# Kernel optimization log

Hardware: AMD Instinct MI355X
Metric: run time of the kernel (lower is better)

Reference implementation:

```python
import jax, jax.numpy as jnp
import numpy as np

SCALE = 128.0  # init arg; divisor is sqrt(scale)
NEG_BIG = -1e10

def setup_inputs() -> dict:
    key = jax.random.key(0)
    kq, kk, kv, km = jax.random.split(key, 4)
    B, Nq, Nk, D = 16, 2048, 2048, 128
    q = jax.random.normal(kq, (B, Nq, D), dtype=jnp.float32)
    k = jax.random.normal(kk, (B, Nk, D), dtype=jnp.float32)
    v = jax.random.normal(kv, (B, Nk, D), dtype=jnp.float32)
    mask = jax.random.randint(km, (B, Nq, Nk), 0, 2).astype(bool)
    return {"q": q, "k": k, "v": v, "mask": mask}

def reference(q, k, v, mask):
    inv = 1.0 / np.sqrt(SCALE).astype(np.float32)
    # scores: [b, q, k]
    scores = jnp.einsum('bqd,bkd->bqk', q, k) * inv
    scores = jnp.where(mask, NEG_BIG, scores)
    att = jax.nn.softmax(scores, axis=-1)
    context = jnp.einsum('bqk,bkd->bqd', att, v)
    return (context, att)
```

## Files before the change

### kernel.cpp

```cpp
#include <hip/hip_runtime.h>

#define B_ 16
#define NQ 2048
#define NK 2048
#define DH 128
#define INV 0.08838834764831843f

typedef __attribute__((ext_vector_type(8))) short bf16x8;
typedef __attribute__((ext_vector_type(4))) float f32x4;

__device__ __forceinline__ unsigned short f2b(float f) {
  unsigned u = __float_as_uint(f);
  u += 0x7fff + ((u >> 16) & 1);
  return (unsigned short)(u >> 16);
}

__global__ __launch_bounds__(256) void k_cvt(
    const float* __restrict__ src, unsigned short* __restrict__ dst, int n4) {
  int i = blockIdx.x * 256 + threadIdx.x;
  if (i >= n4) return;
  float4 f = ((const float4*)src)[i];
  ushort4 u;
  u.x = f2b(f.x); u.y = f2b(f.y); u.z = f2b(f.z); u.w = f2b(f.w);
  ((ushort4*)dst)[i] = u;
}

__global__ __launch_bounds__(256) void k_trans(
    const float* __restrict__ v, unsigned short* __restrict__ vt) {
  __shared__ float tile[32][33];
  const int b = blockIdx.z, kv0 = blockIdx.x << 5, d0 = blockIdx.y << 5;
  const int tx = threadIdx.x & 31, ty = threadIdx.x >> 5;
  #pragma unroll
  for (int i = 0; i < 4; i++)
    tile[ty + 8*i][tx] = v[((size_t)b*NK + kv0 + ty + 8*i)*DH + d0 + tx];
  __syncthreads();
  #pragma unroll
  for (int i = 0; i < 4; i++)
    vt[((size_t)b*DH + d0 + ty + 8*i)*NK + kv0 + tx] = f2b(tile[tx][ty + 8*i]);
}

__global__ __launch_bounds__(256) void k_attn(
    const unsigned short* __restrict__ qb, const unsigned short* __restrict__ kb,
    const unsigned short* __restrict__ vtb, const int* __restrict__ mask,
    float* __restrict__ att, float* __restrict__ ctx) {
  __shared__ unsigned short Qs[64][136];
  __shared__ unsigned short Ks[64][136];
  __shared__ unsigned short Vs[128][72];
  __shared__ unsigned short Ps[64][72];
  __shared__ unsigned int   Mb[64][65];
  __shared__ float Lrow[64];

  const int t = threadIdx.x;
  const int wave = t >> 6, lane = t & 63, quad = lane >> 4, l15 = lane & 15;
  const int b = blockIdx.y, q0 = blockIdx.x << 6;
  const int qh = wave >> 1, nh = wave & 1;

  const unsigned short* qg = qb  + ((size_t)b*NQ + q0)*DH;
  const unsigned short* kg = kb  + (size_t)b*NK*DH;
  const unsigned short* vg = vtb + (size_t)b*DH*NK;
  const int*   mg   = mask + ((size_t)b*NQ + q0)*NK;
  float*       attg = att  + ((size_t)b*NQ + q0)*NK;

  {
    int r = t >> 2, c = (t & 3) << 5;
    const unsigned short* src = qg + (size_t)r*DH + c;
    #pragma unroll
    for (int i = 0; i < 4; i++)
      *(uint4*)&Qs[r][c + 8*i] = *(const uint4*)(src + 8*i);
  }
  if (t < 64) Lrow[t] = 0.f;

  float lsum[8] = {0,0,0,0,0,0,0,0};

  for (int k0 = 0; k0 < NK; k0 += 64) {
    int mreg[2][2][4];
    #pragma unroll
    for (int mt = 0; mt < 2; mt++)
      #pragma unroll
      for (int nt = 0; nt < 2; nt++)
        #pragma unroll
        for (int r = 0; r < 4; r++) {
          int row = qh*32 + mt*16 + quad*4 + r;
          int col = k0 + nh*32 + nt*16 + l15;
          mreg[mt][nt][r] = mg[(size_t)row*NK + col];
        }
    __syncthreads();
    { int r = t >> 2, c = (t & 3) << 5;
      const unsigned short* src = kg + (size_t)(k0 + r)*DH + c;
      #pragma unroll
      for (int i = 0; i < 4; i++)
        *(uint4*)&Ks[r][c + 8*i] = *(const uint4*)(src + 8*i);
    }
    __syncthreads();
    f32x4 sa00 = 0, sa01 = 0, sa10 = 0, sa11 = 0;
    #pragma unroll
    for (int kd = 0; kd < 4; kd++) {
      bf16x8 a0 = *(const bf16x8*)&Qs[qh*32      + l15][kd*32 + quad*8];
      bf16x8 a1 = *(const bf16x8*)&Qs[qh*32 + 16 + l15][kd*32 + quad*8];
      bf16x8 b0 = *(const bf16x8*)&Ks[nh*32      + l15][kd*32 + quad*8];
      bf16x8 b1 = *(const bf16x8*)&Ks[nh*32 + 16 + l15][kd*32 + quad*8];
      sa00 = __builtin_amdgcn_mfma_f32_16x16x32_bf16(a0, b0, sa00, 0, 0, 0);
      sa01 = __builtin_amdgcn_mfma_f32_16x16x32_bf16(a0, b1, sa01, 0, 0, 0);
      sa10 = __builtin_amdgcn_mfma_f32_16x16x32_bf16(a1, b0, sa10, 0, 0, 0);
      sa11 = __builtin_amdgcn_mfma_f32_16x16x32_bf16(a1, b1, sa11, 0, 0, 0);
    }
    #pragma unroll
    for (int mt = 0; mt < 2; mt++)
      #pragma unroll
      for (int nt = 0; nt < 2; nt++) {
        const f32x4 s = mt ? (nt ? sa11 : sa10) : (nt ? sa01 : sa00);
        #pragma unroll
        for (int r = 0; r < 4; r++) {
          bool mm = mreg[mt][nt][r] != 0;
          unsigned long long bal = __ballot(mm);
          if (l15 == 0) {
            int row = qh*32 + mt*16 + quad*4 + r;
            ((unsigned short*)&Mb[0][0])[row*130 + (k0>>4) + nh*2 + nt] =
                (unsigned short)(bal >> (quad*16));
          }
          float p = mm ? 0.f : __expf(s[r]*INV);
          lsum[mt*4 + r] += p;
        }
      }
  }
  __syncthreads();
  #pragma unroll
  for (int j = 0; j < 8; j++)
    atomicAdd(&Lrow[qh*32 + (j>>2)*16 + quad*4 + (j&3)], lsum[j]);
  __syncthreads();
  float il[8];
  #pragma unroll
  for (int j = 0; j < 8; j++)
    il[j] = 1.0f / Lrow[qh*32 + (j>>2)*16 + quad*4 + (j&3)];

  f32x4 ca[2][4];
  #pragma unroll
  for (int i = 0; i < 2; i++)
    #pragma unroll
    for (int j = 0; j < 4; j++) ca[i][j] = 0;

  for (int k0 = 0; k0 < NK; k0 += 64) {
    __syncthreads();
    { int r = t >> 2, c = (t & 3) << 5;
      const unsigned short* src = kg + (size_t)(k0 + r)*DH + c;
      #pragma unroll
      for (int i = 0; i < 4; i++)
        *(uint4*)&Ks[r][c + 8*i] = *(const uint4*)(src + 8*i);
      int d = t >> 1, c2 = (t & 1) << 5;
      const unsigned short* vsrc = vg + (size_t)d*NK + k0 + c2;
      #pragma unroll
      for (int i = 0; i < 4; i++)
        *(uint4*)&Vs[d][c2 + 8*i] = *(const uint4*)(vsrc + 8*i);
    }
    __syncthreads();
    f32x4 sa00 = 0, sa01 = 0, sa10 = 0, sa11 = 0;
    #pragma unroll
    for (int kd = 0; kd < 4; kd++) {
      bf16x8 a0 = *(const bf16x8*)&Qs[qh*32      + l15][kd*32 + quad*8];
      bf16x8 a1 = *(const bf16x8*)&Qs[qh*32 + 16 + l15][kd*32 + quad*8];
      bf16x8 b0 = *(const bf16x8*)&Ks[nh*32      + l15][kd*32 + quad*8];
      bf16x8 b1 = *(const bf16x8*)&Ks[nh*32 + 16 + l15][kd*32 + quad*8];
      sa00 = __builtin_amdgcn_mfma_f32_16x16x32_bf16(a0, b0, sa00, 0, 0, 0);
      sa01 = __builtin_amdgcn_mfma_f32_16x16x32_bf16(a0, b1, sa01, 0, 0, 0);
      sa10 = __builtin_amdgcn_mfma_f32_16x16x32_bf16(a1, b0, sa10, 0, 0, 0);
      sa11 = __builtin_amdgcn_mfma_f32_16x16x32_bf16(a1, b1, sa11, 0, 0, 0);
    }
    #pragma unroll
    for (int mt = 0; mt < 2; mt++)
      #pragma unroll
      for (int nt = 0; nt < 2; nt++) {
        const f32x4 s = mt ? (nt ? sa11 : sa10) : (nt ? sa01 : sa00);
        #pragma unroll
        for (int r = 0; r < 4; r++) {
          int row  = qh*32 + mt*16 + quad*4 + r;
          int coll = nh*32 + nt*16 + l15;
          unsigned w = Mb[row][(k0>>5) + nh];
          int bit = (w >> (nt*16 + l15)) & 1;
          float p = bit ? 0.f : __expf(s[r]*INV) * il[mt*4 + r];
          attg[(size_t)row*NK + k0 + coll] = p;
          Ps[row][coll] = f2b(p);
        }
      }
    __syncthreads();
    #pragma unroll
    for (int kv = 0; kv < 2; kv++) {
      bf16x8 pa0 = *(const bf16x8*)&Ps[qh*32      + l15][kv*32 + quad*8];
      bf16x8 pa1 = *(const bf16x8*)&Ps[qh*32 + 16 + l15][kv*32 + quad*8];
      #pragma unroll
      for (int dt = 0; dt < 4; dt++) {
        bf16x8 vb = *(const bf16x8*)&Vs[nh*64 + dt*16 + l15][kv*32 + quad*8];
        ca[0][dt] = __builtin_amdgcn_mfma_f32_16x16x32_bf16(pa0, vb, ca[0][dt], 0, 0, 0);
        ca[1][dt] = __builtin_amdgcn_mfma_f32_16x16x32_bf16(pa1, vb, ca[1][dt], 0, 0, 0);
      }
    }
  }

  float* cg = ctx + ((size_t)b*NQ + q0)*DH;
  #pragma unroll
  for (int mt = 0; mt < 2; mt++)
    #pragma unroll
    for (int dt = 0; dt < 4; dt++)
      #pragma unroll
      for (int r = 0; r < 4; r++) {
        int row = qh*32 + mt*16 + quad*4 + r;
        int col = nh*64 + dt*16 + l15;
        cg[(size_t)row*DH + col] = ca[mt][dt][r];
      }
}

extern "C" void kernel_launch(void* const* d_in, const int* in_sizes, int n_in,
                              void* d_out, int out_size, void* d_ws, size_t ws_size,
                              hipStream_t stream) {
  const float* q = (const float*)d_in[0];
  const float* k = (const float*)d_in[1];
  const float* v = (const float*)d_in[2];
  const int* mask = (const int*)d_in[3];
  float* ctx = (float*)d_out;
  float* att = ctx + (size_t)B_*NQ*DH;

  const size_t NE = (size_t)B_*NQ*DH;
  unsigned short* qws = (unsigned short*)d_ws;
  unsigned short* kws = qws + NE;
  unsigned short* vws = kws + NE;

  k_cvt  <<<(int)(NE/1024), 256, 0, stream>>>(q, qws, (int)(NE/4));
  k_cvt  <<<(int)(NE/1024), 256, 0, stream>>>(k, kws, (int)(NE/4));
  k_trans<<<dim3(NK/32, DH/32, B_), 256, 0, stream>>>(v, vws);
  k_attn <<<dim3(NQ/64, B_), 256, 0, stream>>>(qws, kws, vws, mask, att, ctx);
}
```

Baseline: 603.2 us.

## Pipeline attention kernel with async global-to-LDS loads, swizzled LDS and smaller query tiles

Rewrites the attention kernel to use 32-row query tiles and keep Q fragments in registers. K and V tiles are staged into XOR-swizzled LDS via global_load_lds and double-buffered with explicit vmcnt waits, so loads overlap the MFMA work. The mask bits are packed into shift registers instead of an LDS bitmap, and mask loads and att stores become nontemporal. It also remaps block IDs for locality, raises occupancy via launch bounds, and adds setprio around the MFMAs. Hand-written waitcnt and barrier sequencing adds correctness risk.

```diff
diff --git a/kernel.cpp b/kernel.cpp
--- a/kernel.cpp
+++ b/kernel.cpp
@@ -9,10 +9,17 @@
 typedef __attribute__((ext_vector_type(8))) short bf16x8;
 typedef __attribute__((ext_vector_type(4))) float f32x4;
 
+typedef const __attribute__((address_space(1))) unsigned int* gas1_t;
+typedef __attribute__((address_space(3))) unsigned int* las3_t;
+
 __device__ __forceinline__ unsigned short f2b(float f) {
   unsigned u = __float_as_uint(f);
   u += 0x7fff + ((u >> 16) & 1);
   return (unsigned short)(u >> 16);
+}
+
+__device__ __forceinline__ void gl_lds16(const unsigned short* g, unsigned short* l) {
+  __builtin_amdgcn_global_load_lds((gas1_t)g, (las3_t)l, 16, 0, 0);
 }
 
 __global__ __launch_bounds__(256) void k_cvt(
@@ -39,173 +46,209 @@
     vt[((size_t)b*DH + d0 + ty + 8*i)*NK + kv0 + tx] = f2b(tile[tx][ty + 8*i]);
 }
 
-__global__ __launch_bounds__(256) void k_attn(
+__global__ __launch_bounds__(256, 4) void k_attn(
     const unsigned short* __restrict__ qb, const unsigned short* __restrict__ kb,
     const unsigned short* __restrict__ vtb, const int* __restrict__ mask,
     float* __restrict__ att, float* __restrict__ ctx) {
-  __shared__ unsigned short Qs[64][136];
-  __shared__ unsigned short Ks[64][136];
-  __shared__ unsigned short Vs[128][72];
-  __shared__ unsigned short Ps[64][72];
-  __shared__ unsigned int   Mb[64][65];
-  __shared__ float Lrow[64];
+  __shared__ unsigned short KA[64*128];
+  __shared__ unsigned short VA[128*64];
+  __shared__ unsigned short Ps[32*64];
+  __shared__ float Lrow[32];
 
   const int t = threadIdx.x;
   const int wave = t >> 6, lane = t & 63, quad = lane >> 4, l15 = lane & 15;
-  const int b = blockIdx.y, q0 = blockIdx.x << 6;
-  const int qh = wave >> 1, nh = wave & 1;
+  const int rh = wave >> 1, nh = wave & 1;
+
+  const int p = blockIdx.x + (blockIdx.y << 6);
+  const int lid = ((p & 7) << 7) + (p >> 3);
+  const int b = lid >> 6, q0 = (lid & 63) << 5;
 
   const unsigned short* qg = qb  + ((size_t)b*NQ + q0)*DH;
   const unsigned short* kg = kb  + (size_t)b*NK*DH;
   const unsigned short* vg = vtb + (size_t)b*DH*NK;
-  const int*   mg   = mask + ((size_t)b*NQ + q0)*NK;
-  float*       attg = att  + ((size_t)b*NQ + q0)*NK;
-
-  {
-    int r = t >> 2, c = (t & 3) << 5;
-    const unsigned short* src = qg + (size_t)r*DH + c;
-    #pragma unroll
-    for (int i = 0; i < 4; i++)
-      *(uint4*)&Qs[r][c + 8*i] = *(const uint4*)(src + 8*i);
-  }
-  if (t < 64) Lrow[t] = 0.f;
-
-  float lsum[8] = {0,0,0,0,0,0,0,0};
-
-  for (int k0 = 0; k0 < NK; k0 += 64) {
-    int mreg[2][2][4];
-    #pragma unroll
-    for (int mt = 0; mt < 2; mt++)
-      #pragma unroll
-      for (int nt = 0; nt < 2; nt++)
-        #pragma unroll
-        for (int r = 0; r < 4; r++) {
-          int row = qh*32 + mt*16 + quad*4 + r;
-          int col = k0 + nh*32 + nt*16 + l15;
-          mreg[mt][nt][r] = mg[(size_t)row*NK + col];
-        }
-    __syncthreads();
-    { int r = t >> 2, c = (t & 3) << 5;
-      const unsigned short* src = kg + (size_t)(k0 + r)*DH + c;
-      #pragma unroll
-      for (int i = 0; i < 4; i++)
-        *(uint4*)&Ks[r][c + 8*i] = *(const uint4*)(src + 8*i);
-    }
-    __syncthreads();
-    f32x4 sa00 = 0, sa01 = 0, sa10 = 0, sa11 = 0;
+  const int* mg   = mask + ((size_t)b*NQ + q0)*NK;
+  float*     attg = att  + ((size_t)b*NQ + q0)*NK;
+  float*     cg   = ctx  + ((size_t)b*NQ + q0)*DH;
+
+  if (t < 32) Lrow[t] = 0.f;
+
+  bf16x8 qf[4];
+  { const unsigned short* qr = qg + (size_t)(rh*16 + l15)*DH + quad*8;
+    #pragma unroll
+    for (int kd = 0; kd < 4; kd++) qf[kd] = *(const bf16x8*)(qr + kd*32); }
+
+  const int row0 = rh*16 + quad*4;
+  const int* mgR[4]; float* attR[4];
+  #pragma unroll
+  for (int r = 0; r < 4; r++) {
+    mgR[r]  = mg   + (size_t)(row0 + r)*NK + nh*32 + l15;
+    attR[r] = attg + (size_t)(row0 + r)*NK + nh*32 + l15;
+  }
+
+  const int kr0 = nh*32 + l15, kr1 = kr0 + 16;
+  const int kbs0 = (kr0 << 8) ^ ((kr0 & 7) << 4);
+  const int kbs1 = (kr1 << 8) ^ ((kr1 & 7) << 4);
+  const int pr  = rh*16 + l15;
+  const int pbs = (pr << 7) ^ ((pr & 7) << 4);
+  int vbs[4];
+  #pragma unroll
+  for (int dt = 0; dt < 4; dt++) {
+    int d = nh*64 + dt*16 + l15;
+    vbs[dt] = (d << 7) ^ ((d & 7) << 4);
+  }
+
+  auto stageK = [&](unsigned short* buf, const unsigned short* src) {
+    #pragma unroll
+    for (int i = 0; i < 4; i++) {
+      int L = (wave << 12) + (i << 10) + (lane << 4);
+      int row = L >> 8;
+      int cb  = (L & 255) ^ ((row & 7) << 4);
+      gl_lds16(src + ((size_t)row << 7) + (cb >> 1), buf + (L >> 1));
+    }
+  };
+  auto stageV = [&](const unsigned short* src) {
+    #pragma unroll
+    for (int i = 0; i < 4; i++) {
+      int L = (wave << 12) + (i << 10) + (lane << 4);
+      int d  = L >> 7;
+      int cb = (L & 127) ^ ((d & 7) << 4);
+      gl_lds16(src + (size_t)d*NK + (cb >> 1), VA + (L >> 1));
+    }
+  };
+  auto loadMask = [&](int k0, int* mr) {
+    #pragma unroll
+    for (int nt = 0; nt < 2; nt++)
+      #pragma unroll
+      for (int r = 0; r < 4; r++)
+        mr[nt*4 + r] = __builtin_nontemporal_load(mgR[r] + k0 + nt*16);
+  };
+  auto qkt = [&](const unsigned short* buf, f32x4& s0v, f32x4& s1v) {
+    s0v = 0; s1v = 0;
+    const char* bc = (const char*)buf;
+    __builtin_amdgcn_s_setprio(1);
     #pragma unroll
     for (int kd = 0; kd < 4; kd++) {
-      bf16x8 a0 = *(const bf16x8*)&Qs[qh*32      + l15][kd*32 + quad*8];
-      bf16x8 a1 = *(const bf16x8*)&Qs[qh*32 + 16 + l15][kd*32 + quad*8];
-      bf16x8 b0 = *(const bf16x8*)&Ks[nh*32      + l15][kd*32 + quad*8];
-      bf16x8 b1 = *(const bf16x8*)&Ks[nh*32 + 16 + l15][kd*32 + quad*8];
-      sa00 = __builtin_amdgcn_mfma_f32_16x16x32_bf16(a0, b0, sa00, 0, 0, 0);
-      sa01 = __builtin_amdgcn_mfma_f32_16x16x32_bf16(a0, b1, sa01, 0, 0, 0);
-      sa10 = __builtin_amdgcn_mfma_f32_16x16x32_bf16(a1, b0, sa10, 0, 0, 0);
-      sa11 = __builtin_amdgcn_mfma_f32_16x16x32_bf16(a1, b1, sa11, 0, 0, 0);
-    }
-    #pragma unroll
-    for (int mt = 0; mt < 2; mt++)
-      #pragma unroll
-      for (int nt = 0; nt < 2; nt++) {
-        const f32x4 s = mt ? (nt ? sa11 : sa10) : (nt ? sa01 : sa00);
-        #pragma unroll
-        for (int r = 0; r < 4; r++) {
-          bool mm = mreg[mt][nt][r] != 0;
-          unsigned long long bal = __ballot(mm);
-          if (l15 == 0) {
-            int row = qh*32 + mt*16 + quad*4 + r;
-            ((unsigned short*)&Mb[0][0])[row*130 + (k0>>4) + nh*2 + nt] =
-                (unsigned short)(bal >> (quad*16));
-          }
-          float p = mm ? 0.f : __expf(s[r]*INV);
-          lsum[mt*4 + r] += p;
-        }
+      int cb = (kd*32 + quad*8) << 1;
+      bf16x8 b0 = *(const bf16x8*)(bc + (kbs0 ^ cb));
+      bf16x8 b1 = *(const bf16x8*)(bc + (kbs1 ^ cb));
+      s0v = __builtin_amdgcn_mfma_f32_16x16x32_bf16(qf[kd], b0, s0v, 0, 0, 0);
+      s1v = __builtin_amdgcn_mfma_f32_16x16x32_bf16(qf[kd], b1, s1v, 0, 0, 0);
+    }
+    __builtin_amdgcn_s_setprio(0);
+  };
+
+  unsigned mw0=0,mw1=0,mw2=0,mw3=0,mw4=0,mw5=0,mw6=0,mw7=0;
+  float ls[4] = {0.f, 0.f, 0.f, 0.f};
+
+  auto epi1 = [&](const int* mr, const f32x4& s0v, const f32x4& s1v) {
+    unsigned nb = 0;
+    #pragma unroll
+    for (int nt = 0; nt < 2; nt++) {
+      const f32x4& sv = nt ? s1v : s0v;
+      #pragma unroll
+      for (int r = 0; r < 4; r++) {
+        float e = __expf(sv[r]*INV);
+        if (mr[nt*4 + r] != 0) { nb |= 1u << (nt*4 + r); e = 0.f; }
+        ls[r] += e;
       }
-  }
+    }
+    mw0=(mw0>>8)|(mw1<<24); mw1=(mw1>>8)|(mw2<<24); mw2=(mw2>>8)|(mw3<<24);
+    mw3=(mw3>>8)|(mw4<<24); mw4=(mw4>>8)|(mw5<<24); mw5=(mw5>>8)|(mw6<<24);
+    mw6=(mw6>>8)|(mw7<<24); mw7=(mw7>>8)|(nb<<24);
+  };
+
+  int mrA[8], mrB[8];
+  stageK(KA, kg);
+  loadMask(0, mrA);
+
+  for (int t2 = 0; t2 < 32; t2 += 2) {
+    __builtin_amdgcn_s_barrier();
+    asm volatile("" ::: "memory");
+    stageK(VA, kg + (size_t)(t2+1)*64*DH);
+    loadMask((t2+1)*64, mrB);
+    asm volatile("s_waitcnt vmcnt(12)" ::: "memory");
+    __builtin_amdgcn_s_barrier();
+    asm volatile("" ::: "memory");
+    { f32x4 s0, s1; qkt(KA, s0, s1); epi1(mrA, s0, s1); }
+
+    __builtin_amdgcn_s_barrier();
+    asm volatile("" ::: "memory");
+    if (t2 + 2 < 32) {
+      stageK(KA, kg + (size_t)(t2+2)*64*DH);
+      loadMask((t2+2)*64, mrA);
+      asm volatile("s_waitcnt vmcnt(12)" ::: "memory");
+    } else {
+      asm volatile("s_waitcnt vmcnt(0)" ::: "memory");
+    }
+    __builtin_amdgcn_s_barrier();
+    asm volatile("" ::: "memory");
+    { f32x4 s0, s1; qkt(VA, s0, s1); epi1(mrB, s0, s1); }
+  }
+
   __syncthreads();
   #pragma unroll
-  for (int j = 0; j < 8; j++)
-    atomicAdd(&Lrow[qh*32 + (j>>2)*16 + quad*4 + (j&3)], lsum[j]);
+  for (int r = 0; r < 4; r++) atomicAdd(&Lrow[row0 + r], ls[r]);
   __syncthreads();
-  float il[8];
-  #pragma unroll
-  for (int j = 0; j < 8; j++)
-    il[j] = 1.0f / Lrow[qh*32 + (j>>2)*16 + quad*4 + (j&3)];
-
-  f32x4 ca[2][4];
-  #pragma unroll
-  for (int i = 0; i < 2; i++)
-    #pragma unroll
-    for (int j = 0; j < 4; j++) ca[i][j] = 0;
-
-  for (int k0 = 0; k0 < NK; k0 += 64) {
-    __syncthreads();
-    { int r = t >> 2, c = (t & 3) << 5;
-      const unsigned short* src = kg + (size_t)(k0 + r)*DH + c;
-      #pragma unroll
-      for (int i = 0; i < 4; i++)
-        *(uint4*)&Ks[r][c + 8*i] = *(const uint4*)(src + 8*i);
-      int d = t >> 1, c2 = (t & 1) << 5;
-      const unsigned short* vsrc = vg + (size_t)d*NK + k0 + c2;
-      #pragma unroll
-      for (int i = 0; i < 4; i++)
-        *(uint4*)&Vs[d][c2 + 8*i] = *(const uint4*)(vsrc + 8*i);
-    }
-    __syncthreads();
-    f32x4 sa00 = 0, sa01 = 0, sa10 = 0, sa11 = 0;
-    #pragma unroll
-    for (int kd = 0; kd < 4; kd++) {
-      bf16x8 a0 = *(const bf16x8*)&Qs[qh*32      + l15][kd*32 + quad*8];
-      bf16x8 a1 = *(const bf16x8*)&Qs[qh*32 + 16 + l15][kd*32 + quad*8];
-      bf16x8 b0 = *(const bf16x8*)&Ks[nh*32      + l15][kd*32 + quad*8];
-      bf16x8 b1 = *(const bf16x8*)&Ks[nh*32 + 16 + l15][kd*32 + quad*8];
-      sa00 = __builtin_amdgcn_mfma_f32_16x16x32_bf16(a0, b0, sa00, 0, 0, 0);
-      sa01 = __builtin_amdgcn_mfma_f32_16x16x32_bf16(a0, b1, sa01, 0, 0, 0);
-      sa10 = __builtin_amdgcn_mfma_f32_16x16x32_bf16(a1, b0, sa10, 0, 0, 0);
-      sa11 = __builtin_amdgcn_mfma_f32_16x16x32_bf16(a1, b1, sa11, 0, 0, 0);
-    }
-    #pragma unroll
-    for (int mt = 0; mt < 2; mt++)
-      #pragma unroll
-      for (int nt = 0; nt < 2; nt++) {
-        const f32x4 s = mt ? (nt ? sa11 : sa10) : (nt ? sa01 : sa00);
-        #pragma unroll
-        for (int r = 0; r < 4; r++) {
-          int row  = qh*32 + mt*16 + quad*4 + r;
-          int coll = nh*32 + nt*16 + l15;
-          unsigned w = Mb[row][(k0>>5) + nh];
-          int bit = (w >> (nt*16 + l15)) & 1;
-          float p = bit ? 0.f : __expf(s[r]*INV) * il[mt*4 + r];
-          attg[(size_t)row*NK + k0 + coll] = p;
-          Ps[row][coll] = f2b(p);
-        }
+  float il[4];
+  #pragma unroll
+  for (int r = 0; r < 4; r++) il[r] = 1.0f / Lrow[row0 + r];
+
+  f32x4 ca[4];
+  #pragma unroll
+  for (int dt = 0; dt < 4; dt++) ca[dt] = 0;
+
+  stageK(KA, kg);
+  for (int tt = 0; tt < 32; tt++) {
+    __builtin_amdgcn_s_barrier();
+    asm volatile("" ::: "memory");
+    stageV(vg + tt*64);
+    asm volatile("s_waitcnt vmcnt(4)" ::: "memory");
+    __builtin_amdgcn_s_barrier();
+    asm volatile("" ::: "memory");
+    f32x4 s0, s1;
+    qkt(KA, s0, s1);
+
+    unsigned nb = mw0 & 255u;
+    mw0=(mw0>>8)|(mw1<<24); mw1=(mw1>>8)|(mw2<<24); mw2=(mw2>>8)|(mw3<<24);
+    mw3=(mw3>>8)|(mw4<<24); mw4=(mw4>>8)|(mw5<<24); mw5=(mw5>>8)|(mw6<<24);
+    mw6=(mw6>>8)|(mw7<<24); mw7>>=8;
+    #pragma unroll
+    for (int nt = 0; nt < 2; nt++) {
+      const f32x4& sv = nt ? s1 : s0;
+      #pragma unroll
+      for (int r = 0; r < 4; r++) {
+        float e = __expf(sv[r]*INV) * il[r];
+        if ((nb >> (nt*4 + r)) & 1) e = 0.f;
+        __builtin_nontemporal_store(e, attR[r] + tt*64 + nt*16);
+        int row = row0 + r;
+        int cbw = ((nh*32 + nt*16 + l15) << 1) ^ ((row & 7) << 4);
+        *(unsigned short*)((char*)Ps + (row << 7) + cbw) = f2b(e);
       }
-    __syncthreads();
+    }
+    asm volatile("s_waitcnt vmcnt(8) lgkmcnt(0)" ::: "memory");
+    __builtin_amdgcn_s_barrier();
+    asm volatile("" ::: "memory");
+    if (tt + 1 < 32) stageK(KA, kg + (size_t)(tt+1)*64*DH);
+
+    __builtin_amdgcn_s_setprio(1);
     #pragma unroll
     for (int kv = 0; kv < 2; kv++) {
-      bf16x8 pa0 = *(const bf16x8*)&Ps[qh*32      + l15][kv*32 + quad*8];
-      bf16x8 pa1 = *(const bf16x8*)&Ps[qh*32 + 16 + l15][kv*32 + quad*8];
+      int cb = (kv*32 + quad*8) << 1;
+      bf16x8 pa = *(const bf16x8*)((const char*)Ps + (pbs ^ cb));
       #pragma unroll
       for (int dt = 0; dt < 4; dt++) {
-        bf16x8 vb = *(const bf16x8*)&Vs[nh*64 + dt*16 + l15][kv*32 + quad*8];
-        ca[0][dt] = __builtin_amdgcn_mfma_f32_16x16x32_bf16(pa0, vb, ca[0][dt], 0, 0, 0);
-        ca[1][dt] = __builtin_amdgcn_mfma_f32_16x16x32_bf16(pa1, vb, ca[1][dt], 0, 0, 0);
+        bf16x8 vb = *(const bf16x8*)((const char*)VA + (vbs[dt] ^ cb));
+        ca[dt] = __builtin_amdgcn_mfma_f32_16x16x32_bf16(pa, vb, ca[dt], 0, 0, 0);
       }
     }
-  }
-
-  float* cg = ctx + ((size_t)b*NQ + q0)*DH;
-  #pragma unroll
-  for (int mt = 0; mt < 2; mt++)
-    #pragma unroll
-    for (int dt = 0; dt < 4; dt++)
-      #pragma unroll
-      for (int r = 0; r < 4; r++) {
-        int row = qh*32 + mt*16 + quad*4 + r;
-        int col = nh*64 + dt*16 + l15;
-        cg[(size_t)row*DH + col] = ca[mt][dt][r];
-      }
+    __builtin_amdgcn_s_setprio(0);
+  }
+
+  #pragma unroll
+  for (int dt = 0; dt < 4; dt++)
+    #pragma unroll
+    for (int r = 0; r < 4; r++)
+      cg[(size_t)(row0 + r)*DH + nh*64 + dt*16 + l15] = ca[dt][r];
 }
 
 extern "C" void kernel_launch(void* const* d_in, const int* in_sizes, int n_in,
@@ -226,5 +269,5 @@
   k_cvt  <<<(int)(NE/1024), 256, 0, stream>>>(q, qws, (int)(NE/4));
   k_cvt  <<<(int)(NE/1024), 256, 0, stream>>>(k, kws, (int)(NE/4));
   k_trans<<<dim3(NK/32, DH/32, B_), 256, 0, stream>>>(v, vws);
-  k_attn <<<dim3(NQ/64, B_), 256, 0, stream>>>(qws, kws, vws, mask, att, ctx);
-}
+  k_attn <<<dim3(NQ/32, B_), 256, 0, stream>>>(qws, kws, vws, mask, att, ctx);
+}
```

After: 572.5 us. -5.1%, faster.
